# Optimization experiments

Measured on AMD Instinct MI355X. Metric: run time of the kernel, lower is better.

The kernel has to match this reference:

```python
import jax, jax.numpy as jnp
import numpy as np


def setup_inputs() -> dict:
    key = jax.random.key(0)
    k1, k2, k3, k4, k5 = jax.random.split(key, 5)
    B, S, E, T = 64, 2048, 256, 100
    h = jax.random.normal(k1, (B, S, E), dtype=jnp.float32)
    theta = jax.random.uniform(k2, (B, T), dtype=jnp.float32)
    w = jax.random.normal(k3, (E, T), dtype=jnp.float32) * 0.05
    v = jax.random.normal(k4, (E, 1), dtype=jnp.float32) * 0.05
    u = jax.random.normal(k5, (E, E), dtype=jnp.float32) * 0.05
    return {"h": h, "theta": theta, "w": w, "v": v, "u": u}


def reference(h, theta, w, v, u):
    # h: [B,S,E], theta: [B,T], w: [E,T], v: [E,1], u: [E,E]
    theta_w = theta @ w.T                      # [B,E]
    h_u = jnp.einsum('bse,ef->bsf', h, u)      # [B,S,E]
    g = jnp.tanh(theta_w[:, None, :] + h_u) @ v  # [B,S,1]
    weight = jax.nn.softmax(g[..., 0], axis=-1)  # [B,S]
    vec = jnp.einsum('bs,bse->be', weight, h)    # [B,E]
    return vec
```

## Files before the change

### kernel.cpp

```cpp
#include <hip/hip_runtime.h>
#include <hip/hip_bf16.h>
#include <math.h>


#define E_DIM 256
#define GM 64

typedef __bf16 bf16x8 __attribute__((ext_vector_type(8)));
typedef float  f32x4  __attribute__((ext_vector_type(4)));

__device__ __forceinline__ unsigned short f2bf(float x) {
    return __builtin_bit_cast(unsigned short, (__bf16)x);
}
__device__ __forceinline__ float bf2f(unsigned short b) {
    return __builtin_bit_cast(float, (unsigned)b << 16);
}

__device__ __forceinline__ unsigned swz(unsigned byte) {
    return byte ^ ((((byte) >> 9) & 7) << 4);
}

__device__ __forceinline__ float fast_tanh(float x) {
    const float e = __expf(2.0f * x);
    const float r = __builtin_amdgcn_rcpf(e + 1.0f);
    return fmaf(-2.0f, r, 1.0f);
}

__global__ __launch_bounds__(256) void k_transpose(const float* __restrict__ u,
                                                   unsigned short* __restrict__ u_t) {
    const int f = blockIdx.x, e = threadIdx.x;
    u_t[(size_t)f * E_DIM + e] = f2bf(u[(size_t)e * E_DIM + f]);
}

__global__ __launch_bounds__(E_DIM) void k_thetaw(const float* __restrict__ theta,
                                                  const float* __restrict__ w,
                                                  float* __restrict__ tw,
                                                  int T) {
    __shared__ float th[128];
    const int b = blockIdx.x;
    const int e = threadIdx.x;
    if (threadIdx.x < T) th[threadIdx.x] = theta[b * T + threadIdx.x];
    __syncthreads();
    float acc = 0.f;
    for (int t = 0; t < T; ++t) acc = fmaf(th[t], w[e * T + t], acc);
    tw[b * E_DIM + e] = acc;
}

__global__ __launch_bounds__(256, 2) void k_gate_fused(const float* __restrict__ h,
                                                       const unsigned short* __restrict__ u_t,
                                                       const float* __restrict__ tw_,
                                                       const float* __restrict__ v,
                                                       float* __restrict__ partial,
                                                       float* __restrict__ pm,
                                                       float* __restrict__ pd,
                                                       int S, int SC) {
    __shared__ unsigned short h_lds[GM * E_DIM];
    __shared__ float red[4][GM];
    __shared__ float exw[GM];
    __shared__ float pacc[4][E_DIM];

    const int b   = blockIdx.y;
    const int sc  = blockIdx.x;
    const int s0  = sc * GM;
    const int tid = threadIdx.x;
    const int w   = tid >> 6;
    const int l   = tid & 63;
    const int lg  = l >> 4;
    const int lc  = l & 15;
    const int f0w = w * 64;

    bf16x8 ub[8][4];
#pragma unroll
    for (int kt = 0; kt < 8; ++kt)
#pragma unroll
        for (int n = 0; n < 4; ++n)
            ub[kt][n] = *reinterpret_cast<const bf16x8*>(
                u_t + (size_t)(f0w + n * 16 + lc) * E_DIM + kt * 32 + lg * 8);

    const float* hb = h + ((size_t)b * S + s0) * E_DIM;
    char* ldsb = (char*)h_lds;
#pragma unroll
    for (int it = 0; it < 16; ++it) {
        const int row = it * 4 + w;
        const float4 hv = *reinterpret_cast<const float4*>(hb + (size_t)row * E_DIM + l * 4);
        uint2 pk;
        pk.x = (unsigned)f2bf(hv.x) | ((unsigned)f2bf(hv.y) << 16);
        pk.y = (unsigned)f2bf(hv.z) | ((unsigned)f2bf(hv.w) << 16);
        *reinterpret_cast<uint2*>(ldsb + swz(row * 512 + l * 8)) = pk;
    }

    float tw_f[4], v_f[4];
#pragma unroll
    for (int n = 0; n < 4; ++n) {
        const int f = f0w + n * 16 + lc;
        tw_f[n] = tw_[b * E_DIM + f];
        v_f[n]  = v[f];
    }

    f32x4 acc[4][4];
#pragma unroll
    for (int m = 0; m < 4; ++m)
#pragma unroll
        for (int n = 0; n < 4; ++n)
            acc[m][n] = (f32x4){0.f, 0.f, 0.f, 0.f};

    __syncthreads();

#pragma unroll
    for (int kt = 0; kt < 8; ++kt) {
        bf16x8 af[4];
#pragma unroll
        for (int m = 0; m < 4; ++m)
            af[m] = *reinterpret_cast<const bf16x8*>(
                ldsb + swz((m * 16 + lc) * 512 + kt * 64 + lg * 16));
#pragma unroll
        for (int m = 0; m < 4; ++m)
#pragma unroll
            for (int n = 0; n < 4; ++n)
                acc[m][n] = __builtin_amdgcn_mfma_f32_16x16x32_bf16(
                    af[m], ub[kt][n], acc[m][n], 0, 0, 0);
    }

    float part[4][4] = {};
#pragma unroll
    for (int n = 0; n < 4; ++n)
#pragma unroll
        for (int m = 0; m < 4; ++m)
#pragma unroll
            for (int i = 0; i < 4; ++i)
                part[m][i] += fast_tanh(acc[m][n][i] + tw_f[n]) * v_f[n];

#pragma unroll
    for (int off = 1; off < 16; off <<= 1)
#pragma unroll
        for (int m = 0; m < 4; ++m)
#pragma unroll
            for (int i = 0; i < 4; ++i)
                part[m][i] += __shfl_xor(part[m][i], off, 64);

    if (lc == 0) {
#pragma unroll
        for (int m = 0; m < 4; ++m)
#pragma unroll
            for (int i = 0; i < 4; ++i)
                red[w][m * 16 + lg * 4 + i] = part[m][i];
    }
    __syncthreads();

    if (tid < GM) {
        const float g = red[0][tid] + red[1][tid] + red[2][tid] + red[3][tid];
        float mx = g;
#pragma unroll
        for (int off = 1; off < 64; off <<= 1)
            mx = fmaxf(mx, __shfl_xor(mx, off, 64));
        const float ex = __expf(g - mx);
        float d = ex;
#pragma unroll
        for (int off = 1; off < 64; off <<= 1)
            d += __shfl_xor(d, off, 64);
        exw[tid] = ex;
        if (tid == 0) {
            pm[(size_t)b * SC + sc] = mx;
            pd[(size_t)b * SC + sc] = d;
        }
    }
    __syncthreads();

    f32x4 a4 = (f32x4){0.f, 0.f, 0.f, 0.f};
#pragma unroll
    for (int j = 0; j < 16; ++j) {
        const int row = w * 16 + j;
        const float ws = exw[row];
        const uint2 hv = *reinterpret_cast<const uint2*>(ldsb + swz(row * 512 + l * 8));
        a4[0] = fmaf(ws, bf2f((unsigned short)(hv.x & 0xffff)), a4[0]);
        a4[1] = fmaf(ws, bf2f((unsigned short)(hv.x >> 16)),    a4[1]);
        a4[2] = fmaf(ws, bf2f((unsigned short)(hv.y & 0xffff)), a4[2]);
        a4[3] = fmaf(ws, bf2f((unsigned short)(hv.y >> 16)),    a4[3]);
    }
    *reinterpret_cast<f32x4*>(&pacc[w][l * 4]) = a4;
    __syncthreads();

    const float p = pacc[0][tid] + pacc[1][tid] + pacc[2][tid] + pacc[3][tid];
    partial[((size_t)b * SC + sc) * E_DIM + tid] = p;
}

__global__ __launch_bounds__(256) void k_combine(const float* __restrict__ partial,
                                                 const float* __restrict__ pm,
                                                 const float* __restrict__ pd,
                                                 float* __restrict__ out,
                                                 int SC) {
    const int b = blockIdx.x, t = threadIdx.x;
    __shared__ float sm[64], sd[64];
    if (t < SC) {
        sm[t] = pm[(size_t)b * SC + t];
        sd[t] = pd[(size_t)b * SC + t];
    }
    __syncthreads();

    float M = -3.4e38f;
    for (int c = 0; c < SC; ++c) M = fmaxf(M, sm[c]);

    float num = 0.f, den = 0.f;
    for (int c = 0; c < SC; ++c) {
        const float s = __expf(sm[c] - M);
        den = fmaf(s, sd[c], den);
        num = fmaf(s, partial[((size_t)b * SC + c) * E_DIM + t], num);
    }
    out[(size_t)b * E_DIM + t] = num / den;
}

extern "C" void kernel_launch(void* const* d_in, const int* in_sizes, int n_in,
                              void* d_out, int out_size, void* d_ws, size_t ws_size,
                              hipStream_t stream) {
    const float* h     = (const float*)d_in[0];
    const float* theta = (const float*)d_in[1];
    const float* w     = (const float*)d_in[2];
    const float* v     = (const float*)d_in[3];
    const float* u     = (const float*)d_in[4];
    float* out = (float*)d_out;

    const int E = in_sizes[3];
    const int T = in_sizes[2] / E;
    const int B = in_sizes[1] / T;
    const int S = in_sizes[0] / (B * E);
    const int SC = S / GM;

    float* tw = (float*)d_ws;
    unsigned short* u_t = (unsigned short*)(tw + (size_t)B * E);
    float* partial = (float*)(u_t + (size_t)E * E);
    float* pm = partial + (size_t)B * SC * E;
    float* pd = pm + (size_t)B * SC;

    k_transpose<<<dim3(E), dim3(E), 0, stream>>>(u, u_t);
    k_thetaw<<<dim3(B), dim3(E), 0, stream>>>(theta, w, tw, T);
    k_gate_fused<<<dim3(SC, B), dim3(256), 0, stream>>>(h, u_t, tw, v, partial, pm, pd, S, SC);
    k_combine<<<dim3(B), dim3(256), 0, stream>>>(partial, pm, pd, out, SC);
}
```

Baseline: 64.34 us.

## Process four chunks per block with double-buffered LDS prefetch of next h tile

Each gate block now handles NC=4 consecutive 64-row chunks. The bf16 u fragments are loaded into registers once and reused across all four chunks. While the MFMA work runs on the current LDS buffer, the next chunk's h rows are loaded from global memory and written into a second LDS buffer, so load latency overlaps compute. The cost is a smaller grid (512 blocks instead of 2048), doubled LDS use (64 KB for the two h buffers) and higher register pressure, which may reduce occupancy.

Measured after the change: 124.2 us. 93.0% more time.

```diff
diff --git a/kernel.cpp b/kernel.cpp
--- a/kernel.cpp
+++ b/kernel.cpp
@@ -5,6 +5,7 @@
 
 #define E_DIM 256
 #define GM 64
+#define NC 4
 
 typedef __bf16 bf16x8 __attribute__((ext_vector_type(8)));
 typedef float  f32x4  __attribute__((ext_vector_type(4)));
@@ -54,14 +55,13 @@
                                                        float* __restrict__ pm,
                                                        float* __restrict__ pd,
                                                        int S, int SC) {
-    __shared__ unsigned short h_lds[GM * E_DIM];
+    __shared__ unsigned short h_lds[2][GM * E_DIM];
     __shared__ float red[4][GM];
     __shared__ float exw[GM];
     __shared__ float pacc[4][E_DIM];
 
     const int b   = blockIdx.y;
-    const int sc  = blockIdx.x;
-    const int s0  = sc * GM;
+    const int sc0 = blockIdx.x * NC;
     const int tid = threadIdx.x;
     const int w   = tid >> 6;
     const int l   = tid & 63;
@@ -77,16 +77,20 @@
             ub[kt][n] = *reinterpret_cast<const bf16x8*>(
                 u_t + (size_t)(f0w + n * 16 + lc) * E_DIM + kt * 32 + lg * 8);
 
-    const float* hb = h + ((size_t)b * S + s0) * E_DIM;
-    char* ldsb = (char*)h_lds;
-#pragma unroll
-    for (int it = 0; it < 16; ++it) {
-        const int row = it * 4 + w;
-        const float4 hv = *reinterpret_cast<const float4*>(hb + (size_t)row * E_DIM + l * 4);
-        uint2 pk;
-        pk.x = (unsigned)f2bf(hv.x) | ((unsigned)f2bf(hv.y) << 16);
-        pk.y = (unsigned)f2bf(hv.z) | ((unsigned)f2bf(hv.w) << 16);
-        *reinterpret_cast<uint2*>(ldsb + swz(row * 512 + l * 8)) = pk;
+    {
+        const float* hb = h + ((size_t)b * S + sc0 * GM) * E_DIM;
+        char* ldsb = (char*)h_lds[0];
+        float4 st[16];
+#pragma unroll
+        for (int it = 0; it < 16; ++it)
+            st[it] = *reinterpret_cast<const float4*>(hb + (size_t)(it * 4 + w) * E_DIM + l * 4);
+#pragma unroll
+        for (int it = 0; it < 16; ++it) {
+            uint2 pk;
+            pk.x = (unsigned)f2bf(st[it].x) | ((unsigned)f2bf(st[it].y) << 16);
+            pk.y = (unsigned)f2bf(st[it].z) | ((unsigned)f2bf(st[it].w) << 16);
+            *reinterpret_cast<uint2*>(ldsb + swz((it * 4 + w) * 512 + l * 8)) = pk;
+        }
     }
 
     float tw_f[4], v_f[4];
@@ -97,91 +101,121 @@
         v_f[n]  = v[f];
     }
 
-    f32x4 acc[4][4];
-#pragma unroll
-    for (int m = 0; m < 4; ++m)
+    __syncthreads();
+
+    for (int c = 0; c < NC; ++c) {
+        const int sc = sc0 + c;
+        char* cur = (char*)h_lds[c & 1];
+        char* nxt = (char*)h_lds[(c & 1) ^ 1];
+        const float* hbn = h + ((size_t)b * S + (sc + 1) * GM) * E_DIM;
+        const bool prefetch = (c < NC - 1);
+
+        f32x4 acc[4][4];
+#pragma unroll
+        for (int m = 0; m < 4; ++m)
+#pragma unroll
+            for (int n = 0; n < 4; ++n)
+                acc[m][n] = (f32x4){0.f, 0.f, 0.f, 0.f};
+
+#pragma unroll
+        for (int q = 0; q < 4; ++q) {
+            float4 st[4];
+            if (prefetch) {
+#pragma unroll
+                for (int j = 0; j < 4; ++j) {
+                    const int row = q * 16 + j * 4 + w;
+                    st[j] = *reinterpret_cast<const float4*>(hbn + (size_t)row * E_DIM + l * 4);
+                }
+            }
+#pragma unroll
+            for (int kk = 0; kk < 2; ++kk) {
+                const int kt = q * 2 + kk;
+                bf16x8 af[4];
+#pragma unroll
+                for (int m = 0; m < 4; ++m)
+                    af[m] = *reinterpret_cast<const bf16x8*>(
+                        cur + swz((m * 16 + lc) * 512 + kt * 64 + lg * 16));
+#pragma unroll
+                for (int m = 0; m < 4; ++m)
+#pragma unroll
+                    for (int n = 0; n < 4; ++n)
+                        acc[m][n] = __builtin_amdgcn_mfma_f32_16x16x32_bf16(
+                            af[m], ub[kt][n], acc[m][n], 0, 0, 0);
+            }
+            if (prefetch) {
+#pragma unroll
+                for (int j = 0; j < 4; ++j) {
+                    const int row = q * 16 + j * 4 + w;
+                    uint2 pk;
+                    pk.x = (unsigned)f2bf(st[j].x) | ((unsigned)f2bf(st[j].y) << 16);
+                    pk.y = (unsigned)f2bf(st[j].z) | ((unsigned)f2bf(st[j].w) << 16);
+                    *reinterpret_cast<uint2*>(nxt + swz(row * 512 + l * 8)) = pk;
+                }
+            }
+        }
+
+        float part[4][4] = {};
 #pragma unroll
         for (int n = 0; n < 4; ++n)
-            acc[m][n] = (f32x4){0.f, 0.f, 0.f, 0.f};
-
-    __syncthreads();
-
-#pragma unroll
-    for (int kt = 0; kt < 8; ++kt) {
-        bf16x8 af[4];
-#pragma unroll
-        for (int m = 0; m < 4; ++m)
-            af[m] = *reinterpret_cast<const bf16x8*>(
-                ldsb + swz((m * 16 + lc) * 512 + kt * 64 + lg * 16));
-#pragma unroll
-        for (int m = 0; m < 4; ++m)
-#pragma unroll
-            for (int n = 0; n < 4; ++n)
-                acc[m][n] = __builtin_amdgcn_mfma_f32_16x16x32_bf16(
-                    af[m], ub[kt][n], acc[m][n], 0, 0, 0);
-    }
-
-    float part[4][4] = {};
-#pragma unroll
-    for (int n = 0; n < 4; ++n)
-#pragma unroll
-        for (int m = 0; m < 4; ++m)
-#pragma unroll
-            for (int i = 0; i < 4; ++i)
-                part[m][i] += fast_tanh(acc[m][n][i] + tw_f[n]) * v_f[n];
-
-#pragma unroll
-    for (int off = 1; off < 16; off <<= 1)
-#pragma unroll
-        for (int m = 0; m < 4; ++m)
-#pragma unroll
-            for (int i = 0; i < 4; ++i)
-                part[m][i] += __shfl_xor(part[m][i], off, 64);
-
-    if (lc == 0) {
-#pragma unroll
-        for (int m = 0; m < 4; ++m)
-#pragma unroll
-            for (int i = 0; i < 4; ++i)
-                red[w][m * 16 + lg * 4 + i] = part[m][i];
-    }
-    __syncthreads();
-
-    if (tid < GM) {
-        const float g = red[0][tid] + red[1][tid] + red[2][tid] + red[3][tid];
-        float mx = g;
-#pragma unroll
-        for (int off = 1; off < 64; off <<= 1)
-            mx = fmaxf(mx, __shfl_xor(mx, off, 64));
-        const float ex = __expf(g - mx);
-        float d = ex;
-#pragma unroll
-        for (int off = 1; off < 64; off <<= 1)
-            d += __shfl_xor(d, off, 64);
-        exw[tid] = ex;
-        if (tid == 0) {
-            pm[(size_t)b * SC + sc] = mx;
-            pd[(size_t)b * SC + sc] = d;
-        }
-    }
-    __syncthreads();
-
-    f32x4 a4 = (f32x4){0.f, 0.f, 0.f, 0.f};
-#pragma unroll
-    for (int j = 0; j < 16; ++j) {
-        const int row = w * 16 + j;
-        const float ws = exw[row];
-        const uint2 hv = *reinterpret_cast<const uint2*>(ldsb + swz(row * 512 + l * 8));
-        a4[0] = fmaf(ws, bf2f((unsigned short)(hv.x & 0xffff)), a4[0]);
-        a4[1] = fmaf(ws, bf2f((unsigned short)(hv.x >> 16)),    a4[1]);
-        a4[2] = fmaf(ws, bf2f((unsigned short)(hv.y & 0xffff)), a4[2]);
-        a4[3] = fmaf(ws, bf2f((unsigned short)(hv.y >> 16)),    a4[3]);
-    }
-    *reinterpret_cast<f32x4*>(&pacc[w][l * 4]) = a4;
-    __syncthreads();
-
-    const float p = pacc[0][tid] + pacc[1][tid] + pacc[2][tid] + pacc[3][tid];
-    partial[((size_t)b * SC + sc) * E_DIM + tid] = p;
+#pragma unroll
+            for (int m = 0; m < 4; ++m)
+#pragma unroll
+                for (int i = 0; i < 4; ++i)
+                    part[m][i] += fast_tanh(acc[m][n][i] + tw_f[n]) * v_f[n];
+
+#pragma unroll
+        for (int off = 1; off < 16; off <<= 1)
+#pragma unroll
+            for (int m = 0; m < 4; ++m)
+#pragma unroll
+                for (int i = 0; i < 4; ++i)
+                    part[m][i] += __shfl_xor(part[m][i], off, 64);
+
+        if (lc == 0) {
+#pragma unroll
+            for (int m = 0; m < 4; ++m)
+#pragma unroll
+                for (int i = 0; i < 4; ++i)
+                    red[w][m * 16 + lg * 4 + i] = part[m][i];
+        }
+        __syncthreads();
+
+        if (tid < GM) {
+            const float g = red[0][tid] + red[1][tid] + red[2][tid] + red[3][tid];
+            float mx = g;
+#pragma unroll
+            for (int off = 1; off < 64; off <<= 1)
+                mx = fmaxf(mx, __shfl_xor(mx, off, 64));
+            const float ex = __expf(g - mx);
+            float d = ex;
+#pragma unroll
+            for (int off = 1; off < 64; off <<= 1)
+                d += __shfl_xor(d, off, 64);
+            exw[tid] = ex;
+            if (tid == 0) {
+                pm[(size_t)b * SC + sc] = mx;
+                pd[(size_t)b * SC + sc] = d;
+            }
+        }
+        __syncthreads();
+
+        f32x4 a4 = (f32x4){0.f, 0.f, 0.f, 0.f};
+#pragma unroll
+        for (int j = 0; j < 16; ++j) {
+            const int row = w * 16 + j;
+            const float ws = exw[row];
+            const uint2 hv = *reinterpret_cast<const uint2*>(cur + swz(row * 512 + l * 8));
+            a4[0] = fmaf(ws, bf2f((unsigned short)(hv.x & 0xffff)), a4[0]);
+            a4[1] = fmaf(ws, bf2f((unsigned short)(hv.x >> 16)),    a4[1]);
+            a4[2] = fmaf(ws, bf2f((unsigned short)(hv.y & 0xffff)), a4[2]);
+            a4[3] = fmaf(ws, bf2f((unsigned short)(hv.y >> 16)),    a4[3]);
+        }
+        *reinterpret_cast<f32x4*>(&pacc[w][l * 4]) = a4;
+        __syncthreads();
+
+        const float p = pacc[0][tid] + pacc[1][tid] + pacc[2][tid] + pacc[3][tid];
+        partial[((size_t)b * SC + sc) * E_DIM + tid] = p;
+    }
 }
 
 __global__ __launch_bounds__(256) void k_combine(const float* __restrict__ partial,
@@ -233,6 +267,6 @@
 
     k_transpose<<<dim3(E), dim3(E), 0, stream>>>(u, u_t);
     k_thetaw<<<dim3(B), dim3(E), 0, stream>>>(theta, w, tw, T);
-    k_gate_fused<<<dim3(SC, B), dim3(256), 0, stream>>>(h, u_t, tw, v, partial, pm, pd, S, SC);
+    k_gate_fused<<<dim3(SC / NC, B), dim3(256), 0, stream>>>(h, u_t, tw, v, partial, pm, pd, S, SC);
     k_combine<<<dim3(B), dim3(256), 0, stream>>>(partial, pm, pd, out, SC);
 }
```

## Halve gate tile rows and stream U fragments to raise occupancy

Applied to the files above, without the earlier changes.

Shrinks the per-block sequence tile from 64 to 32 rows and raises the launch-bounds occupancy target from 2 to 4 blocks per CU. The U weight fragments are no longer held entirely in registers; instead two k-slices are double-buffered and reloaded from global memory inside the k loop. The aim is to cut register and LDS pressure so more waves can hide the latency of the h stream. In exchange, U is re-read from cache twice as often overall, and the partial-result buffer and the combine pass double in size.

Measured after the change: 88.67 us. +37.8%, slower.

```diff
diff --git a/kernel.cpp b/kernel.cpp
--- a/kernel.cpp
+++ b/kernel.cpp
@@ -4,7 +4,7 @@
 
 
 #define E_DIM 256
-#define GM 64
+#define GM 32
 
 typedef __bf16 bf16x8 __attribute__((ext_vector_type(8)));
 typedef float  f32x4  __attribute__((ext_vector_type(4)));
@@ -46,7 +46,7 @@
     tw[b * E_DIM + e] = acc;
 }
 
-__global__ __launch_bounds__(256, 2) void k_gate_fused(const float* __restrict__ h,
+__global__ __launch_bounds__(256, 4) void k_gate_fused(const float* __restrict__ h,
                                                        const unsigned short* __restrict__ u_t,
                                                        const float* __restrict__ tw_,
                                                        const float* __restrict__ v,
@@ -61,7 +61,6 @@
 
     const int b   = blockIdx.y;
     const int sc  = blockIdx.x;
-    const int s0  = sc * GM;
     const int tid = threadIdx.x;
     const int w   = tid >> 6;
     const int l   = tid & 63;
@@ -69,18 +68,20 @@
     const int lc  = l & 15;
     const int f0w = w * 64;
 
-    bf16x8 ub[8][4];
-#pragma unroll
-    for (int kt = 0; kt < 8; ++kt)
-#pragma unroll
-        for (int n = 0; n < 4; ++n)
-            ub[kt][n] = *reinterpret_cast<const bf16x8*>(
-                u_t + (size_t)(f0w + n * 16 + lc) * E_DIM + kt * 32 + lg * 8);
-
-    const float* hb = h + ((size_t)b * S + s0) * E_DIM;
+    const unsigned short* ubase = u_t + (size_t)(f0w + lc) * E_DIM + lg * 8;
+
+    bf16x8 ua[4], ub2[4];
+#pragma unroll
+    for (int n = 0; n < 4; ++n)
+        ua[n] = *reinterpret_cast<const bf16x8*>(ubase + n * 16 * E_DIM);
+#pragma unroll
+    for (int n = 0; n < 4; ++n)
+        ub2[n] = *reinterpret_cast<const bf16x8*>(ubase + n * 16 * E_DIM + 32);
+
+    const float* hb = h + ((size_t)b * S + sc * GM) * E_DIM;
     char* ldsb = (char*)h_lds;
 #pragma unroll
-    for (int it = 0; it < 16; ++it) {
+    for (int it = 0; it < 8; ++it) {
         const int row = it * 4 + w;
         const float4 hv = *reinterpret_cast<const float4*>(hb + (size_t)row * E_DIM + l * 4);
         uint2 pk;
@@ -97,35 +98,58 @@
         v_f[n]  = v[f];
     }
 
-    f32x4 acc[4][4];
-#pragma unroll
-    for (int m = 0; m < 4; ++m)
+    f32x4 acc[2][4];
+#pragma unroll
+    for (int m = 0; m < 2; ++m)
 #pragma unroll
         for (int n = 0; n < 4; ++n)
             acc[m][n] = (f32x4){0.f, 0.f, 0.f, 0.f};
 
     __syncthreads();
 
-#pragma unroll
-    for (int kt = 0; kt < 8; ++kt) {
-        bf16x8 af[4];
-#pragma unroll
-        for (int m = 0; m < 4; ++m)
-            af[m] = *reinterpret_cast<const bf16x8*>(
-                ldsb + swz((m * 16 + lc) * 512 + kt * 64 + lg * 16));
-#pragma unroll
-        for (int m = 0; m < 4; ++m)
-#pragma unroll
-            for (int n = 0; n < 4; ++n)
-                acc[m][n] = __builtin_amdgcn_mfma_f32_16x16x32_bf16(
-                    af[m], ub[kt][n], acc[m][n], 0, 0, 0);
-    }
-
-    float part[4][4] = {};
+    for (int kt4 = 0; kt4 < 4; ++kt4) {
+        const int kt0 = kt4 * 2, kt1 = kt4 * 2 + 1;
+        {
+            bf16x8 af0 = *reinterpret_cast<const bf16x8*>(
+                ldsb + swz((0 * 16 + lc) * 512 + kt0 * 64 + lg * 16));
+            bf16x8 af1 = *reinterpret_cast<const bf16x8*>(
+                ldsb + swz((1 * 16 + lc) * 512 + kt0 * 64 + lg * 16));
+#pragma unroll
+            for (int n = 0; n < 4; ++n) {
+                acc[0][n] = __builtin_amdgcn_mfma_f32_16x16x32_bf16(af0, ua[n], acc[0][n], 0, 0, 0);
+                acc[1][n] = __builtin_amdgcn_mfma_f32_16x16x32_bf16(af1, ua[n], acc[1][n], 0, 0, 0);
+            }
+            if (kt4 < 3) {
+#pragma unroll
+                for (int n = 0; n < 4; ++n)
+                    ua[n] = *reinterpret_cast<const bf16x8*>(
+                        ubase + n * 16 * E_DIM + (kt0 + 2) * 32);
+            }
+        }
+        {
+            bf16x8 af0 = *reinterpret_cast<const bf16x8*>(
+                ldsb + swz((0 * 16 + lc) * 512 + kt1 * 64 + lg * 16));
+            bf16x8 af1 = *reinterpret_cast<const bf16x8*>(
+                ldsb + swz((1 * 16 + lc) * 512 + kt1 * 64 + lg * 16));
+#pragma unroll
+            for (int n = 0; n < 4; ++n) {
+                acc[0][n] = __builtin_amdgcn_mfma_f32_16x16x32_bf16(af0, ub2[n], acc[0][n], 0, 0, 0);
+                acc[1][n] = __builtin_amdgcn_mfma_f32_16x16x32_bf16(af1, ub2[n], acc[1][n], 0, 0, 0);
+            }
+            if (kt4 < 3) {
+#pragma unroll
+                for (int n = 0; n < 4; ++n)
+                    ub2[n] = *reinterpret_cast<const bf16x8*>(
+                        ubase + n * 16 * E_DIM + (kt1 + 2) * 32);
+            }
+        }
+    }
+
+    float part[2][4] = {};
 #pragma unroll
     for (int n = 0; n < 4; ++n)
 #pragma unroll
-        for (int m = 0; m < 4; ++m)
+        for (int m = 0; m < 2; ++m)
 #pragma unroll
             for (int i = 0; i < 4; ++i)
                 part[m][i] += fast_tanh(acc[m][n][i] + tw_f[n]) * v_f[n];
@@ -133,14 +157,14 @@
 #pragma unroll
     for (int off = 1; off < 16; off <<= 1)
 #pragma unroll
-        for (int m = 0; m < 4; ++m)
+        for (int m = 0; m < 2; ++m)
 #pragma unroll
             for (int i = 0; i < 4; ++i)
                 part[m][i] += __shfl_xor(part[m][i], off, 64);
 
     if (lc == 0) {
 #pragma unroll
-        for (int m = 0; m < 4; ++m)
+        for (int m = 0; m < 2; ++m)
 #pragma unroll
             for (int i = 0; i < 4; ++i)
                 red[w][m * 16 + lg * 4 + i] = part[m][i];
@@ -151,12 +175,12 @@
         const float g = red[0][tid] + red[1][tid] + red[2][tid] + red[3][tid];
         float mx = g;
 #pragma unroll
-        for (int off = 1; off < 64; off <<= 1)
+        for (int off = 1; off < 32; off <<= 1)
             mx = fmaxf(mx, __shfl_xor(mx, off, 64));
         const float ex = __expf(g - mx);
         float d = ex;
 #pragma unroll
-        for (int off = 1; off < 64; off <<= 1)
+        for (int off = 1; off < 32; off <<= 1)
             d += __shfl_xor(d, off, 64);
         exw[tid] = ex;
         if (tid == 0) {
@@ -168,8 +192,8 @@
 
     f32x4 a4 = (f32x4){0.f, 0.f, 0.f, 0.f};
 #pragma unroll
-    for (int j = 0; j < 16; ++j) {
-        const int row = w * 16 + j;
+    for (int j = 0; j < 8; ++j) {
+        const int row = w * 8 + j;
         const float ws = exw[row];
         const uint2 hv = *reinterpret_cast<const uint2*>(ldsb + swz(row * 512 + l * 8));
         a4[0] = fmaf(ws, bf2f((unsigned short)(hv.x & 0xffff)), a4[0]);
@@ -190,7 +214,7 @@
                                                  float* __restrict__ out,
                                                  int SC) {
     const int b = blockIdx.x, t = threadIdx.x;
-    __shared__ float sm[64], sd[64];
+    __shared__ float sm[128], sd[128];
     if (t < SC) {
         sm[t] = pm[(size_t)b * SC + t];
         sd[t] = pd[(size_t)b * SC + t];
```

## Split gate GEMM from weighted sum, double-buffer h via direct LDS loads

Applied to the files above, without the earlier changes.

The fused gate kernel becomes two kernels. A 512-thread GEMM kernel with 128-row tiles streams fp32 h into double-buffered swizzled LDS using global_load_lds, converts to bf16 in registers and writes the gate scores g. A separate kernel then re-reads h in fp32 to form the softmax-weighted partial sums. The transpose and theta-w prep kernels are merged into one launch. The aim is to overlap h loads with MFMA work and reduce launches, at the cost of reading h (128 MB) from HBM twice instead of once, which likely makes this memory-bound task slower.

New measurement: 99.53 us. +54.7%, slower.

```diff
diff --git a/kernel.cpp b/kernel.cpp
--- a/kernel.cpp
+++ b/kernel.cpp
@@ -4,20 +4,14 @@
 
 
 #define E_DIM 256
-#define GM 64
+#define BM 128
+#define BK 64
 
 typedef __bf16 bf16x8 __attribute__((ext_vector_type(8)));
 typedef float  f32x4  __attribute__((ext_vector_type(4)));
 
 __device__ __forceinline__ unsigned short f2bf(float x) {
     return __builtin_bit_cast(unsigned short, (__bf16)x);
-}
-__device__ __forceinline__ float bf2f(unsigned short b) {
-    return __builtin_bit_cast(float, (unsigned)b << 16);
-}
-
-__device__ __forceinline__ unsigned swz(unsigned byte) {
-    return byte ^ ((((byte) >> 9) & 7) << 4);
 }
 
 __device__ __forceinline__ float fast_tanh(float x) {
@@ -26,73 +20,69 @@
     return fmaf(-2.0f, r, 1.0f);
 }
 
-__global__ __launch_bounds__(256) void k_transpose(const float* __restrict__ u,
-                                                   unsigned short* __restrict__ u_t) {
-    const int f = blockIdx.x, e = threadIdx.x;
-    u_t[(size_t)f * E_DIM + e] = f2bf(u[(size_t)e * E_DIM + f]);
-}
-
-__global__ __launch_bounds__(E_DIM) void k_thetaw(const float* __restrict__ theta,
-                                                  const float* __restrict__ w,
-                                                  float* __restrict__ tw,
-                                                  int T) {
-    __shared__ float th[128];
-    const int b = blockIdx.x;
-    const int e = threadIdx.x;
-    if (threadIdx.x < T) th[threadIdx.x] = theta[b * T + threadIdx.x];
-    __syncthreads();
-    float acc = 0.f;
-    for (int t = 0; t < T; ++t) acc = fmaf(th[t], w[e * T + t], acc);
-    tw[b * E_DIM + e] = acc;
-}
-
-__global__ __launch_bounds__(256, 2) void k_gate_fused(const float* __restrict__ h,
-                                                       const unsigned short* __restrict__ u_t,
-                                                       const float* __restrict__ tw_,
-                                                       const float* __restrict__ v,
-                                                       float* __restrict__ partial,
-                                                       float* __restrict__ pm,
-                                                       float* __restrict__ pd,
-                                                       int S, int SC) {
-    __shared__ unsigned short h_lds[GM * E_DIM];
-    __shared__ float red[4][GM];
-    __shared__ float exw[GM];
-    __shared__ float pacc[4][E_DIM];
+__global__ __launch_bounds__(256) void k_prep(const float* __restrict__ u,
+                                              const float* __restrict__ theta,
+                                              const float* __restrict__ w,
+                                              unsigned short* __restrict__ u_t,
+                                              float* __restrict__ tw,
+                                              int T) {
+    if (blockIdx.x < E_DIM) {
+        const int f = blockIdx.x, e = threadIdx.x;
+        u_t[(size_t)f * E_DIM + e] = f2bf(u[(size_t)e * E_DIM + f]);
+    } else {
+        __shared__ float th[128];
+        const int b = blockIdx.x - E_DIM;
+        const int e = threadIdx.x;
+        if (threadIdx.x < T) th[threadIdx.x] = theta[b * T + threadIdx.x];
+        __syncthreads();
+        float acc = 0.f;
+        for (int t = 0; t < T; ++t) acc = fmaf(th[t], w[e * T + t], acc);
+        tw[b * E_DIM + e] = acc;
+    }
+}
+
+__global__ __launch_bounds__(512, 2) void k_gate(const float* __restrict__ h,
+                                                 const unsigned short* __restrict__ u_t,
+                                                 const float* __restrict__ tw_,
+                                                 const float* __restrict__ v,
+                                                 float* __restrict__ g,
+                                                 int S) {
+    __shared__ float Abuf[2][BM * BK];
+    __shared__ float red[4][BM];
 
     const int b   = blockIdx.y;
-    const int sc  = blockIdx.x;
-    const int s0  = sc * GM;
+    const int bm  = blockIdx.x;
     const int tid = threadIdx.x;
     const int w   = tid >> 6;
     const int l   = tid & 63;
     const int lg  = l >> 4;
     const int lc  = l & 15;
-    const int f0w = w * 64;
-
-    bf16x8 ub[8][4];
-#pragma unroll
-    for (int kt = 0; kt < 8; ++kt)
-#pragma unroll
-        for (int n = 0; n < 4; ++n)
-            ub[kt][n] = *reinterpret_cast<const bf16x8*>(
-                u_t + (size_t)(f0w + n * 16 + lc) * E_DIM + kt * 32 + lg * 8);
-
-    const float* hb = h + ((size_t)b * S + s0) * E_DIM;
-    char* ldsb = (char*)h_lds;
-#pragma unroll
-    for (int it = 0; it < 16; ++it) {
-        const int row = it * 4 + w;
-        const float4 hv = *reinterpret_cast<const float4*>(hb + (size_t)row * E_DIM + l * 4);
-        uint2 pk;
-        pk.x = (unsigned)f2bf(hv.x) | ((unsigned)f2bf(hv.y) << 16);
-        pk.y = (unsigned)f2bf(hv.z) | ((unsigned)f2bf(hv.w) << 16);
-        *reinterpret_cast<uint2*>(ldsb + swz(row * 512 + l * 8)) = pk;
+    const int nw  = w & 3;
+    const int mw  = w >> 2;
+
+    const float* hb = h + ((size_t)b * S + (size_t)bm * BM) * E_DIM;
+
+    const int srow  = tid >> 4;
+    const int sslot = tid & 15;
+#define STAGE(buf, ks)                                                          \
+    {                                                                           \
+        _Pragma("unroll")                                                       \
+        for (int r = 0; r < 4; ++r) {                                           \
+            const int row = r * 32 + srow;                                      \
+            const char* src = (const char*)(hb + (size_t)row * E_DIM + (ks) * BK) \
+                              + ((sslot ^ (row & 15)) * 16);                    \
+            __builtin_amdgcn_global_load_lds(                                   \
+                (const __attribute__((address_space(1))) void*)src,             \
+                (__attribute__((address_space(3))) void*)                       \
+                    ((char*)Abuf[buf] + r * 8192 + (tid >> 6) * 1024),          \
+                16, 0, 0);                                                      \
+        }                                                                       \
     }
 
     float tw_f[4], v_f[4];
 #pragma unroll
     for (int n = 0; n < 4; ++n) {
-        const int f = f0w + n * 16 + lc;
+        const int f = nw * 64 + n * 16 + lc;
         tw_f[n] = tw_[b * E_DIM + f];
         v_f[n]  = v[f];
     }
@@ -104,84 +94,125 @@
         for (int n = 0; n < 4; ++n)
             acc[m][n] = (f32x4){0.f, 0.f, 0.f, 0.f};
 
-    __syncthreads();
-
-#pragma unroll
-    for (int kt = 0; kt < 8; ++kt) {
-        bf16x8 af[4];
+    STAGE(0, 0);
+    __syncthreads();
+
+#pragma unroll
+    for (int ks = 0; ks < 4; ++ks) {
+        if (ks < 3) STAGE((ks + 1) & 1, ks + 1);
+
+        bf16x8 bn[4][2];
+#pragma unroll
+        for (int n = 0; n < 4; ++n)
+#pragma unroll
+            for (int kt = 0; kt < 2; ++kt)
+                bn[n][kt] = *reinterpret_cast<const bf16x8*>(
+                    u_t + (size_t)(nw * 64 + n * 16 + lc) * E_DIM + ks * BK + kt * 32 + lg * 8);
+
+        const char* base = (const char*)Abuf[ks & 1];
+#pragma unroll
+        for (int kt = 0; kt < 2; ++kt) {
+#pragma unroll
+            for (int m = 0; m < 4; ++m) {
+                const int row = mw * 64 + m * 16 + lc;
+                const unsigned s0 = (unsigned)((kt * 8 + lg * 2) ^ (row & 15));
+                const unsigned s1 = (unsigned)((kt * 8 + lg * 2 + 1) ^ (row & 15));
+                const f32x4 fa0 = *reinterpret_cast<const f32x4*>(base + row * 256 + s0 * 16);
+                const f32x4 fa1 = *reinterpret_cast<const f32x4*>(base + row * 256 + s1 * 16);
+                bf16x8 af;
+#pragma unroll
+                for (int j = 0; j < 4; ++j) {
+                    af[j]     = (__bf16)fa0[j];
+                    af[4 + j] = (__bf16)fa1[j];
+                }
+#pragma unroll
+                for (int n = 0; n < 4; ++n)
+                    acc[m][n] = __builtin_amdgcn_mfma_f32_16x16x32_bf16(
+                        af, bn[n][kt], acc[m][n], 0, 0, 0);
+            }
+        }
+        __syncthreads();
+    }
+
+    float rs[4][4] = {};
+#pragma unroll
+    for (int n = 0; n < 4; ++n)
 #pragma unroll
         for (int m = 0; m < 4; ++m)
-            af[m] = *reinterpret_cast<const bf16x8*>(
-                ldsb + swz((m * 16 + lc) * 512 + kt * 64 + lg * 16));
+#pragma unroll
+            for (int i = 0; i < 4; ++i)
+                rs[m][i] += fast_tanh(acc[m][n][i] + tw_f[n]) * v_f[n];
+
+#pragma unroll
+    for (int off = 1; off < 16; off <<= 1)
 #pragma unroll
         for (int m = 0; m < 4; ++m)
 #pragma unroll
-            for (int n = 0; n < 4; ++n)
-                acc[m][n] = __builtin_amdgcn_mfma_f32_16x16x32_bf16(
-                    af[m], ub[kt][n], acc[m][n], 0, 0, 0);
-    }
-
-    float part[4][4] = {};
-#pragma unroll
-    for (int n = 0; n < 4; ++n)
+            for (int i = 0; i < 4; ++i)
+                rs[m][i] += __shfl_xor(rs[m][i], off, 64);
+
+    if (lc == 0) {
 #pragma unroll
         for (int m = 0; m < 4; ++m)
 #pragma unroll
             for (int i = 0; i < 4; ++i)
-                part[m][i] += fast_tanh(acc[m][n][i] + tw_f[n]) * v_f[n];
-
-#pragma unroll
-    for (int off = 1; off < 16; off <<= 1)
-#pragma unroll
-        for (int m = 0; m < 4; ++m)
-#pragma unroll
-            for (int i = 0; i < 4; ++i)
-                part[m][i] += __shfl_xor(part[m][i], off, 64);
-
-    if (lc == 0) {
-#pragma unroll
-        for (int m = 0; m < 4; ++m)
-#pragma unroll
-            for (int i = 0; i < 4; ++i)
-                red[w][m * 16 + lg * 4 + i] = part[m][i];
-    }
-    __syncthreads();
-
-    if (tid < GM) {
-        const float g = red[0][tid] + red[1][tid] + red[2][tid] + red[3][tid];
-        float mx = g;
+                red[nw][mw * 64 + m * 16 + lg * 4 + i] = rs[m][i];
+    }
+    __syncthreads();
+
+    if (tid < BM)
+        g[(size_t)b * S + (size_t)bm * BM + tid] =
+            red[0][tid] + red[1][tid] + red[2][tid] + red[3][tid];
+#undef STAGE
+}
+
+__global__ __launch_bounds__(256) void k_wsum(const float* __restrict__ h,
+                                              const float* __restrict__ g,
+                                              float* __restrict__ partial,
+                                              float* __restrict__ pm,
+                                              float* __restrict__ pd,
+                                              int S, int SC) {
+    const int b = blockIdx.y, c = blockIdx.x;
+    const int tid = threadIdx.x, w = tid >> 6, l = tid & 63;
+    __shared__ float exw[64];
+    __shared__ float pacc[4][E_DIM];
+
+    if (tid < 64) {
+        const float gv = g[(size_t)b * S + (size_t)c * 64 + tid];
+        float mx = gv;
 #pragma unroll
         for (int off = 1; off < 64; off <<= 1)
             mx = fmaxf(mx, __shfl_xor(mx, off, 64));
-        const float ex = __expf(g - mx);
+        const float ex = __expf(gv - mx);
         float d = ex;
 #pragma unroll
         for (int off = 1; off < 64; off <<= 1)
             d += __shfl_xor(d, off, 64);
         exw[tid] = ex;
         if (tid == 0) {
-            pm[(size_t)b * SC + sc] = mx;
-            pd[(size_t)b * SC + sc] = d;
+            pm[(size_t)b * SC + c] = mx;
+            pd[(size_t)b * SC + c] = d;
         }
     }
     __syncthreads();
 
+    const float* hb = h + ((size_t)b * S + (size_t)c * 64) * E_DIM;
     f32x4 a4 = (f32x4){0.f, 0.f, 0.f, 0.f};
-#pragma unroll
+#pragma unroll 4
     for (int j = 0; j < 16; ++j) {
-        const int row = w * 16 + j;
-        const float ws = exw[row];
-        const uint2 hv = *reinterpret_cast<const uint2*>(ldsb + swz(row * 512 + l * 8));
-        a4[0] = fmaf(ws, bf2f((unsigned short)(hv.x & 0xffff)), a4[0]);
-        a4[1] = fmaf(ws, bf2f((unsigned short)(hv.x >> 16)),    a4[1]);
-        a4[2] = fmaf(ws, bf2f((unsigned short)(hv.y & 0xffff)), a4[2]);
-        a4[3] = fmaf(ws, bf2f((unsigned short)(hv.y >> 16)),    a4[3]);
+        const int s = w * 16 + j;
+        const float ws = exw[s];
+        const f32x4 hv = *reinterpret_cast<const f32x4*>(hb + (size_t)s * E_DIM + l * 4);
+        a4[0] = fmaf(ws, hv[0], a4[0]);
+        a4[1] = fmaf(ws, hv[1], a4[1]);
+        a4[2] = fmaf(ws, hv[2], a4[2]);
+        a4[3] = fmaf(ws, hv[3], a4[3]);
     }
     *reinterpret_cast<f32x4*>(&pacc[w][l * 4]) = a4;
     __syncthreads();
 
-    const float p = pacc[0][tid] + pacc[1][tid] + pacc[2][tid] + pacc[3][tid];
-    partial[((size_t)b * SC + sc) * E_DIM + tid] = p;
+    partial[((size_t)b * SC + c) * E_DIM + tid] =
+        pacc[0][tid] + pacc[1][tid] + pacc[2][tid] + pacc[3][tid];
 }
 
 __global__ __launch_bounds__(256) void k_combine(const float* __restrict__ partial,
@@ -223,16 +254,17 @@
     const int T = in_sizes[2] / E;
     const int B = in_sizes[1] / T;
     const int S = in_sizes[0] / (B * E);
-    const int SC = S / GM;
+    const int SC = S / 64;
 
     float* tw = (float*)d_ws;
     unsigned short* u_t = (unsigned short*)(tw + (size_t)B * E);
-    float* partial = (float*)(u_t + (size_t)E * E);
+    float* g = (float*)(u_t + (size_t)E * E);
+    float* partial = g + (size_t)B * S;
     float* pm = partial + (size_t)B * SC * E;
     float* pd = pm + (size_t)B * SC;
 
-    k_transpose<<<dim3(E), dim3(E), 0, stream>>>(u, u_t);
-    k_thetaw<<<dim3(B), dim3(E), 0, stream>>>(theta, w, tw, T);
-    k_gate_fused<<<dim3(SC, B), dim3(256), 0, stream>>>(h, u_t, tw, v, partial, pm, pd, S, SC);
+    k_prep<<<dim3(E + B), dim3(256), 0, stream>>>(u, theta, w, u_t, tw, T);
+    k_gate<<<dim3(S / BM, B), dim3(512), 0, stream>>>(h, u_t, tw, v, g, S);
+    k_wsum<<<dim3(SC, B), dim3(256), 0, stream>>>(h, g, partial, pm, pd, S, SC);
     k_combine<<<dim3(B), dim3(256), 0, stream>>>(partial, pm, pd, out, SC);
 }
```
